# Kernel optimization log

Measured on AMD Instinct MI355X. Metric: run time of the kernel, lower is better.

Reference implementation:

```python
import jax, jax.numpy as jnp
import numpy as np

B, S, E, H, SN, LMAX = 128, 512, 768, 16, 100, 5
DH = E // H  # 48

def setup_inputs() -> dict:
    key = jax.random.key(0)
    ks = jax.random.split(key, 10)
    idx = jax.random.randint(ks[0], (B, LMAX), 0, S)
    lengths = jax.random.randint(ks[1], (B,), 1, LMAX + 1)
    valid = jnp.arange(LMAX)[None, :] < lengths[:, None]
    locations = jnp.where(valid, idx, -1)
    return {
        "last_hidden_state": jax.random.normal(ks[2], (B, S, E), jnp.float32),
        "sense_emb": jax.random.normal(ks[3], (B, SN, E), jnp.float32),
        "locations": locations,
        "in_proj_weight": jax.random.normal(ks[4], (3 * E, E), jnp.float32) * 0.02,
        "in_proj_bias": jax.random.normal(ks[5], (3 * E,), jnp.float32) * 0.02,
        "out_proj_weight": jax.random.normal(ks[6], (E, E), jnp.float32) * 0.02,
        "out_proj_bias": jax.random.normal(ks[7], (E,), jnp.float32) * 0.02,
        "linear_weight": jax.random.normal(ks[8], (SN, E), jnp.float32) * 0.02,
        "linear_bias": jax.random.normal(ks[9], (SN,), jnp.float32) * 0.02,
    }

def reference(last_hidden_state, sense_emb, locations, in_proj_weight, in_proj_bias,
              out_proj_weight, out_proj_bias, linear_weight, linear_bias):
    # Ragged gather + mean over the valid (non -1) token locations per row.
    mask = (locations != -1)                                   # [B, LMAX]
    safe = jnp.where(mask, locations, 0)                       # [B, LMAX]
    gathered = jnp.take_along_axis(last_hidden_state, safe[..., None], axis=1)  # [B,LMAX,E]
    cnt = mask.sum(axis=1, keepdims=True).astype(last_hidden_state.dtype)
    pun = (gathered * mask[..., None]).sum(axis=1) / cnt       # [B, E]

    # qkv: prepend pun-word embedding to the sense embeddings -> [B, SN+1, E]
    qkv = jnp.concatenate([pun[:, None, :], sense_emb], axis=1)

    # nn.MultiheadAttention with batch_first=False: axis0 = seq (L=B), axis1 = batch (N=SN+1).
    proj = qkv @ in_proj_weight.T + in_proj_bias               # [L, N, 3E]
    q, k, v = jnp.split(proj, 3, axis=-1)
    L, N = qkv.shape[0], qkv.shape[1]
    q = q.reshape(L, N, H, DH) * (DH ** -0.5)
    k = k.reshape(L, N, H, DH)
    v = v.reshape(L, N, H, DH)
    scores = jnp.einsum('lnhd,mnhd->nhlm', q, k)               # [N,H,L,L]
    attn = jax.nn.softmax(scores, axis=-1)
    ctx = jnp.einsum('nhlm,mnhd->lnhd', attn, v).reshape(L, N, E)
    attn_out = ctx @ out_proj_weight.T + out_proj_bias         # [L, N, E]

    res = attn_out[:, 0, :]                                    # [B, E] (batch slot 0)
    res = res @ linear_weight.T + linear_bias                  # [B, SN]
    return res
```

## Files before the change

### kernel.cpp

```cpp
#include <hip/hip_runtime.h>

#define SEQ   512
#define EMB   768
#define K3E   2304
#define NH    16
#define DHD   48

__global__ __launch_bounds__(256) void gemm1_fused(
    const float* __restrict__ lhs, const int* __restrict__ loc,
    const float* __restrict__ Bw, const float* __restrict__ bias,
    float* __restrict__ C)
{
  __shared__ float lds[15360];
  const int t  = threadIdx.x;
  const int w  = t >> 6, l = t & 63;
  const int bm = blockIdx.y * 16, bn = blockIdx.x * 64;
  const int tx = l & 15, ty = l >> 4;
  const int gm = l & 15, gq = l >> 4;
  const int kbase = w * 192;
  const int AW = w * 2816;
  const int BW = w * 2816 + 640;

  int locs[5]; int cnt = 0;
#pragma unroll
  for (int j = 0; j < 5; j++) {
    int v = loc[(bm + gm) * 5 + j];
    locs[j] = v; if (v >= 0) cnt++;
  }
  const float ginv = 1.0f / (float)cnt;
  const float* lrow = lhs + (size_t)(bm + gm) * SEQ * EMB;
  const float* brow = Bw + (size_t)(bn + l) * EMB;

  float4 aF, bF0, bF1, bF2, bF3;

#define G1_LOAD(s) {                                                          \
    int k0 = kbase + (s) * 16;                                                \
    float sx=0.f, sy=0.f, sz=0.f, sw=0.f;                                     \
    _Pragma("unroll")                                                         \
    for (int j = 0; j < 5; j++) {                                             \
      int v = locs[j] >= 0 ? locs[j] : 0;                                     \
      float4 wv = *(const float4*)&lrow[(size_t)v * EMB + k0 + gq * 4];       \
      if (locs[j] >= 0) { sx+=wv.x; sy+=wv.y; sz+=wv.z; sw+=wv.w; }           \
    }                                                                         \
    aF = make_float4(sx*ginv, sy*ginv, sz*ginv, sw*ginv);                     \
    bF0 = *(const float4*)&brow[k0 + 0];                                      \
    bF1 = *(const float4*)&brow[k0 + 4];                                      \
    bF2 = *(const float4*)&brow[k0 + 8];                                      \
    bF3 = *(const float4*)&brow[k0 + 12]; }

#define G1_WRITE(b) {                                                         \
    int Ab = AW + (b) * 320;                                                  \
    lds[Ab + (gq*4+0)*20 + gm] = aF.x;                                        \
    lds[Ab + (gq*4+1)*20 + gm] = aF.y;                                        \
    lds[Ab + (gq*4+2)*20 + gm] = aF.z;                                        \
    lds[Ab + (gq*4+3)*20 + gm] = aF.w;                                        \
    int Bb = BW + (b) * 1088;                                                 \
    lds[Bb +  0*68 + l] = bF0.x; lds[Bb +  1*68 + l] = bF0.y;                 \
    lds[Bb +  2*68 + l] = bF0.z; lds[Bb +  3*68 + l] = bF0.w;                 \
    lds[Bb +  4*68 + l] = bF1.x; lds[Bb +  5*68 + l] = bF1.y;                 \
    lds[Bb +  6*68 + l] = bF1.z; lds[Bb +  7*68 + l] = bF1.w;                 \
    lds[Bb +  8*68 + l] = bF2.x; lds[Bb +  9*68 + l] = bF2.y;                 \
    lds[Bb + 10*68 + l] = bF2.z; lds[Bb + 11*68 + l] = bF2.w;                 \
    lds[Bb + 12*68 + l] = bF3.x; lds[Bb + 13*68 + l] = bF3.y;                 \
    lds[Bb + 14*68 + l] = bF3.z; lds[Bb + 15*68 + l] = bF3.w; }

  float acc[4][4] = {};
  G1_LOAD(0); G1_WRITE(0);
  for (int s = 0; s < 12; s++) {
    int b = s & 1;
    if (s < 11) G1_LOAD(s + 1);
    int Ab = AW + b * 320, Bb = BW + b * 1088;
#pragma unroll
    for (int kk = 0; kk < 16; kk++) {
      float4 a  = *(float4*)&lds[Ab + kk * 20 + ty * 4];
      float4 bb = *(float4*)&lds[Bb + kk * 68 + tx * 4];
      acc[0][0] += a.x*bb.x; acc[0][1] += a.x*bb.y; acc[0][2] += a.x*bb.z; acc[0][3] += a.x*bb.w;
      acc[1][0] += a.y*bb.x; acc[1][1] += a.y*bb.y; acc[1][2] += a.y*bb.z; acc[1][3] += a.y*bb.w;
      acc[2][0] += a.z*bb.x; acc[2][1] += a.z*bb.y; acc[2][2] += a.z*bb.z; acc[2][3] += a.z*bb.w;
      acc[3][0] += a.w*bb.x; acc[3][1] += a.w*bb.y; acc[3][2] += a.w*bb.z; acc[3][3] += a.w*bb.w;
    }
    if (s < 11) G1_WRITE(b ^ 1);
  }

  int Rb = 11264 + w * 1024;
#pragma unroll
  for (int i = 0; i < 4; i++)
    *(float4*)&lds[Rb + (ty*4 + i) * 64 + tx * 4] =
        make_float4(acc[i][0], acc[i][1], acc[i][2], acc[i][3]);
  __syncthreads();
  int o = t * 4;
  int m = o >> 6, n = o & 63;
  float4 s0 = *(float4*)&lds[11264 + 0*1024 + o];
  float4 s1 = *(float4*)&lds[11264 + 1*1024 + o];
  float4 s2 = *(float4*)&lds[11264 + 2*1024 + o];
  float4 s3 = *(float4*)&lds[11264 + 3*1024 + o];
  float4 bb = *(const float4*)&bias[bn + n];
  float4 r = make_float4(s0.x+s1.x+s2.x+s3.x+bb.x, s0.y+s1.y+s2.y+s3.y+bb.y,
                         s0.z+s1.z+s2.z+s3.z+bb.z, s0.w+s1.w+s2.w+s3.w+bb.w);
  *(float4*)&C[(size_t)(bm + m) * K3E + bn + n] = r;
#undef G1_LOAD
#undef G1_WRITE
}

__global__ __launch_bounds__(256) void gemm_red(
    const float* __restrict__ A, const float* __restrict__ Bw,
    const float* __restrict__ bias, float* __restrict__ C,
    int N, int LDC)
{
  __shared__ float lds[9216];
  const int t  = threadIdx.x;
  const int w  = t >> 6, l = t & 63;
  const int bm = blockIdx.y * 16, bn = blockIdx.x * 32;
  const int tx = l & 7, ty = l >> 3;
  const int am = l & 15, aq = l >> 4;
  const int bl = l & 31, bh = l >> 5;
  const int kbase = w * 192;
  const int AW = w * 1792;
  const int BW = w * 1792 + 640;

  const float* arow = A + (size_t)(bm + am) * EMB;
  const int brg = bn + bl;
  const bool bok = brg < N;
  const float* brow = Bw + (size_t)(bok ? brg : (N - 1)) * EMB;

  float4 aF, bF0, bF1;

#define G2_LOAD(s) {                                                          \
    int k0 = kbase + (s) * 16;                                                \
    aF = *(const float4*)&arow[k0 + aq * 4];                                  \
    if (bok) {                                                                \
      bF0 = *(const float4*)&brow[k0 + bh * 8 + 0];                           \
      bF1 = *(const float4*)&brow[k0 + bh * 8 + 4];                           \
    } else {                                                                  \
      bF0 = make_float4(0.f,0.f,0.f,0.f); bF1 = bF0;                          \
    } }

#define G2_WRITE(b) {                                                         \
    int Ab = AW + (b) * 320;                                                  \
    lds[Ab + (aq*4+0)*20 + am] = aF.x;                                        \
    lds[Ab + (aq*4+1)*20 + am] = aF.y;                                        \
    lds[Ab + (aq*4+2)*20 + am] = aF.z;                                        \
    lds[Ab + (aq*4+3)*20 + am] = aF.w;                                        \
    int Bb = BW + (b) * 576;                                                  \
    lds[Bb + (bh*8+0)*36 + bl] = bF0.x; lds[Bb + (bh*8+1)*36 + bl] = bF0.y;   \
    lds[Bb + (bh*8+2)*36 + bl] = bF0.z; lds[Bb + (bh*8+3)*36 + bl] = bF0.w;   \
    lds[Bb + (bh*8+4)*36 + bl] = bF1.x; lds[Bb + (bh*8+5)*36 + bl] = bF1.y;   \
    lds[Bb + (bh*8+6)*36 + bl] = bF1.z; lds[Bb + (bh*8+7)*36 + bl] = bF1.w; }

  float acc[2][4] = {};
  G2_LOAD(0); G2_WRITE(0);
  for (int s = 0; s < 12; s++) {
    int b = s & 1;
    if (s < 11) G2_LOAD(s + 1);
    int Ab = AW + b * 320, Bb = BW + b * 576;
#pragma unroll
    for (int kk = 0; kk < 16; kk++) {
      float2 a  = *(float2*)&lds[Ab + kk * 20 + ty * 2];
      float4 bb = *(float4*)&lds[Bb + kk * 36 + tx * 4];
      acc[0][0] += a.x*bb.x; acc[0][1] += a.x*bb.y; acc[0][2] += a.x*bb.z; acc[0][3] += a.x*bb.w;
      acc[1][0] += a.y*bb.x; acc[1][1] += a.y*bb.y; acc[1][2] += a.y*bb.z; acc[1][3] += a.y*bb.w;
    }
    if (s < 11) G2_WRITE(b ^ 1);
  }

  int Rb = 7168 + w * 512;
#pragma unroll
  for (int i = 0; i < 2; i++)
    *(float4*)&lds[Rb + (ty*2 + i) * 32 + tx * 4] =
        make_float4(acc[i][0], acc[i][1], acc[i][2], acc[i][3]);
  __syncthreads();
  int o = t * 2;
  int m = o >> 5, n = o & 31;
#pragma unroll
  for (int j = 0; j < 2; j++) {
    int ng = bn + n + j;
    if (ng < N) {
      float v = lds[7168 + 0*512 + o + j] + lds[7168 + 1*512 + o + j] +
                lds[7168 + 2*512 + o + j] + lds[7168 + 3*512 + o + j] + bias[ng];
      C[(size_t)(bm + m) * LDC + ng] = v;
    }
  }
#undef G2_LOAD
#undef G2_WRITE
}

__global__ __launch_bounds__(256) void attn_kernel(
    const float* __restrict__ proj, float* __restrict__ ctx)
{
  __shared__ float ks[128][52];
  __shared__ float vs[128][52];
  int h  = blockIdx.x;
  int l0 = blockIdx.y * 16;
  int t  = threadIdx.x;

  for (int i = t; i < 128 * 12; i += 256) {
    int m  = i / 12;
    int dd = (i - m * 12) * 4;
    float4 kv = *(const float4*)&proj[(size_t)m * K3E + EMB     + h * DHD + dd];
    float4 vv = *(const float4*)&proj[(size_t)m * K3E + 2 * EMB + h * DHD + dd];
    *(float4*)&ks[m][dd] = kv;
    *(float4*)&vs[m][dd] = vv;
  }

  int l  = t >> 4;
  int g  = t & 15;
  int lg = l0 + l;
  const float scale = 0.14433756729740643f;
  float q[48];
#pragma unroll
  for (int jj = 0; jj < 12; jj++) {
    float4 qv = *(const float4*)&proj[(size_t)lg * K3E + h * DHD + jj * 4];
    q[jj * 4 + 0] = qv.x * scale; q[jj * 4 + 1] = qv.y * scale;
    q[jj * 4 + 2] = qv.z * scale; q[jj * 4 + 3] = qv.w * scale;
  }
  __syncthreads();

  float sv[8];
  float smax = -1e30f;
#pragma unroll
  for (int jm = 0; jm < 8; jm++) {
    int m = g + jm * 16;
    float s = 0.0f;
#pragma unroll
    for (int dq = 0; dq < 12; dq++) {
      float4 kv = *(const float4*)&ks[m][dq * 4];
      s += q[dq * 4 + 0] * kv.x + q[dq * 4 + 1] * kv.y +
           q[dq * 4 + 2] * kv.z + q[dq * 4 + 3] * kv.w;
    }
    sv[jm] = s;
    smax = fmaxf(smax, s);
  }
#pragma unroll
  for (int off = 1; off < 16; off <<= 1) smax = fmaxf(smax, __shfl_xor(smax, off));
  float ssum = 0.0f;
#pragma unroll
  for (int jm = 0; jm < 8; jm++) { float e = __expf(sv[jm] - smax); sv[jm] = e; ssum += e; }
#pragma unroll
  for (int off = 1; off < 16; off <<= 1) ssum += __shfl_xor(ssum, off);
  float inv = 1.0f / ssum;
#pragma unroll
  for (int jm = 0; jm < 8; jm++) sv[jm] *= inv;

  float acc[48] = {};
#pragma unroll
  for (int jm = 0; jm < 8; jm++) {
    int m = g + jm * 16;
    float p = sv[jm];
#pragma unroll
    for (int dq = 0; dq < 12; dq++) {
      float4 vv = *(const float4*)&vs[m][dq * 4];
      acc[dq * 4 + 0] += p * vv.x; acc[dq * 4 + 1] += p * vv.y;
      acc[dq * 4 + 2] += p * vv.z; acc[dq * 4 + 3] += p * vv.w;
    }
  }

  {
    float buf[24];
    if (g & 8) {
#pragma unroll
      for (int d = 0; d < 24; d++) buf[d] = acc[d];
    } else {
#pragma unroll
      for (int d = 0; d < 24; d++) buf[d] = acc[d + 24];
    }
#pragma unroll
    for (int d = 0; d < 24; d++) buf[d] = __shfl_xor(buf[d], 8);
    if (g & 8) {
#pragma unroll
      for (int d = 0; d < 24; d++) acc[d] = acc[d + 24] + buf[d];
    } else {
#pragma unroll
      for (int d = 0; d < 24; d++) acc[d] = acc[d] + buf[d];
    }
  }
  {
    float buf[12];
    if (g & 4) {
#pragma unroll
      for (int d = 0; d < 12; d++) buf[d] = acc[d];
    } else {
#pragma unroll
      for (int d = 0; d < 12; d++) buf[d] = acc[d + 12];
    }
#pragma unroll
    for (int d = 0; d < 12; d++) buf[d] = __shfl_xor(buf[d], 4);
    if (g & 4) {
#pragma unroll
      for (int d = 0; d < 12; d++) acc[d] = acc[d + 12] + buf[d];
    } else {
#pragma unroll
      for (int d = 0; d < 12; d++) acc[d] = acc[d] + buf[d];
    }
  }
  {
    float buf[6];
    if (g & 2) {
#pragma unroll
      for (int d = 0; d < 6; d++) buf[d] = acc[d];
    } else {
#pragma unroll
      for (int d = 0; d < 6; d++) buf[d] = acc[d + 6];
    }
#pragma unroll
    for (int d = 0; d < 6; d++) buf[d] = __shfl_xor(buf[d], 2);
    if (g & 2) {
#pragma unroll
      for (int d = 0; d < 6; d++) acc[d] = acc[d + 6] + buf[d];
    } else {
#pragma unroll
      for (int d = 0; d < 6; d++) acc[d] = acc[d] + buf[d];
    }
  }
  {
    float buf[3];
    if (g & 1) {
#pragma unroll
      for (int d = 0; d < 3; d++) buf[d] = acc[d];
    } else {
#pragma unroll
      for (int d = 0; d < 3; d++) buf[d] = acc[d + 3];
    }
#pragma unroll
    for (int d = 0; d < 3; d++) buf[d] = __shfl_xor(buf[d], 1);
    if (g & 1) {
#pragma unroll
      for (int d = 0; d < 3; d++) acc[d] = acc[d + 3] + buf[d];
    } else {
#pragma unroll
      for (int d = 0; d < 3; d++) acc[d] = acc[d] + buf[d];
    }
  }
#pragma unroll
  for (int j = 0; j < 3; j++) {
    ctx[(size_t)lg * EMB + h * DHD + g * 3 + j] = acc[j];
  }
}

extern "C" void kernel_launch(void* const* d_in, const int* in_sizes, int n_in,
                              void* d_out, int out_size, void* d_ws, size_t ws_size,
                              hipStream_t stream) {
  const float* lhs   = (const float*)d_in[0];
  const int*   loc   = (const int*)  d_in[2];
  const float* w_in  = (const float*)d_in[3];
  const float* b_in  = (const float*)d_in[4];
  const float* w_out = (const float*)d_in[5];
  const float* b_out = (const float*)d_in[6];
  const float* w_lin = (const float*)d_in[7];
  const float* b_lin = (const float*)d_in[8];
  float* out = (float*)d_out;

  char* ws = (char*)d_ws;
  float* proj     = (float*)(ws);
  float* ctx      = (float*)(ws + 1179648);
  float* attn_out = (float*)(ws + 1179648 + 393216);

  gemm1_fused<<<dim3(36, 8), 256, 0, stream>>>(lhs, loc, w_in, b_in, proj);
  attn_kernel<<<dim3(NH, 8), 256, 0, stream>>>(proj, ctx);
  gemm_red<<<dim3(24, 8), 256, 0, stream>>>(ctx, w_out, b_out, attn_out, EMB, EMB);
  gemm_red<<<dim3(4, 8), 256, 0, stream>>>(attn_out, w_lin, b_lin, out, 100, 100);
}
```

Before: 56.75 us.

## Fold out_proj into final linear and compute combined weight alongside attention

The out-projection and final linear are merged algebraically: Wcomb = W_lin·W_out is computed by extra blocks inside the attention kernel, and the bias W_lin·b_out + b_lin is computed inside the final kernel. This removes one launch and the 128x768x768 out-projection GEMM, replacing it with a 100x768x768 weight product that runs concurrently with attention. The first GEMM's tile width is also halved from 64 to 32 columns, doubling its block count for better CU occupancy. Rounding order changes slightly, and the weight product is recomputed every call.

```diff
diff --git a/kernel.cpp b/kernel.cpp
--- a/kernel.cpp
+++ b/kernel.cpp
@@ -1,25 +1,24 @@
 #include <hip/hip_runtime.h>
 
-#define SEQ   512
-#define EMB   768
-#define K3E   2304
-#define NH    16
-#define DHD   48
-
-__global__ __launch_bounds__(256) void gemm1_fused(
+#define SEQ 512
+#define EMB 768
+#define K3E 2304
+#define DHD 48
+
+__global__ __launch_bounds__(256) void k1_gemm1(
     const float* __restrict__ lhs, const int* __restrict__ loc,
     const float* __restrict__ Bw, const float* __restrict__ bias,
     float* __restrict__ C)
 {
-  __shared__ float lds[15360];
+  __shared__ float lds[7168];
   const int t  = threadIdx.x;
   const int w  = t >> 6, l = t & 63;
-  const int bm = blockIdx.y * 16, bn = blockIdx.x * 64;
-  const int tx = l & 15, ty = l >> 4;
+  const int bm = blockIdx.y * 16, bn = blockIdx.x * 32;
+  const int tx = l & 7, ty = l >> 3;
   const int gm = l & 15, gq = l >> 4;
+  const int bl = l & 31, bh = l >> 5;
   const int kbase = w * 192;
-  const int AW = w * 2816;
-  const int BW = w * 2816 + 640;
+  const int AW = w * 1792, BW = AW + 640;
 
   int locs[5]; int cnt = 0;
 #pragma unroll
@@ -29,85 +28,299 @@
   }
   const float ginv = 1.0f / (float)cnt;
   const float* lrow = lhs + (size_t)(bm + gm) * SEQ * EMB;
-  const float* brow = Bw + (size_t)(bn + l) * EMB;
-
-  float4 aF, bF0, bF1, bF2, bF3;
-
-#define G1_LOAD(s) {                                                          \
-    int k0 = kbase + (s) * 16;                                                \
-    float sx=0.f, sy=0.f, sz=0.f, sw=0.f;                                     \
-    _Pragma("unroll")                                                         \
-    for (int j = 0; j < 5; j++) {                                             \
-      int v = locs[j] >= 0 ? locs[j] : 0;                                     \
-      float4 wv = *(const float4*)&lrow[(size_t)v * EMB + k0 + gq * 4];       \
-      if (locs[j] >= 0) { sx+=wv.x; sy+=wv.y; sz+=wv.z; sw+=wv.w; }           \
-    }                                                                         \
-    aF = make_float4(sx*ginv, sy*ginv, sz*ginv, sw*ginv);                     \
-    bF0 = *(const float4*)&brow[k0 + 0];                                      \
-    bF1 = *(const float4*)&brow[k0 + 4];                                      \
-    bF2 = *(const float4*)&brow[k0 + 8];                                      \
-    bF3 = *(const float4*)&brow[k0 + 12]; }
-
-#define G1_WRITE(b) {                                                         \
-    int Ab = AW + (b) * 320;                                                  \
-    lds[Ab + (gq*4+0)*20 + gm] = aF.x;                                        \
-    lds[Ab + (gq*4+1)*20 + gm] = aF.y;                                        \
-    lds[Ab + (gq*4+2)*20 + gm] = aF.z;                                        \
-    lds[Ab + (gq*4+3)*20 + gm] = aF.w;                                        \
-    int Bb = BW + (b) * 1088;                                                 \
-    lds[Bb +  0*68 + l] = bF0.x; lds[Bb +  1*68 + l] = bF0.y;                 \
-    lds[Bb +  2*68 + l] = bF0.z; lds[Bb +  3*68 + l] = bF0.w;                 \
-    lds[Bb +  4*68 + l] = bF1.x; lds[Bb +  5*68 + l] = bF1.y;                 \
-    lds[Bb +  6*68 + l] = bF1.z; lds[Bb +  7*68 + l] = bF1.w;                 \
-    lds[Bb +  8*68 + l] = bF2.x; lds[Bb +  9*68 + l] = bF2.y;                 \
-    lds[Bb + 10*68 + l] = bF2.z; lds[Bb + 11*68 + l] = bF2.w;                 \
-    lds[Bb + 12*68 + l] = bF3.x; lds[Bb + 13*68 + l] = bF3.y;                 \
-    lds[Bb + 14*68 + l] = bF3.z; lds[Bb + 15*68 + l] = bF3.w; }
-
-  float acc[4][4] = {};
-  G1_LOAD(0); G1_WRITE(0);
+  const float* brow = Bw + (size_t)(bn + bl) * EMB;
+
+  float4 aF, bF0, bF1;
+
+#define K1_LOAD(s) {                                                         \
+    int k0 = kbase + (s) * 16;                                               \
+    float sx=0.f, sy=0.f, sz=0.f, sw=0.f;                                    \
+    _Pragma("unroll")                                                        \
+    for (int j = 0; j < 5; j++) {                                            \
+      int v = locs[j] >= 0 ? locs[j] : 0;                                    \
+      float4 wv = *(const float4*)&lrow[(size_t)v * EMB + k0 + gq * 4];      \
+      if (locs[j] >= 0) { sx+=wv.x; sy+=wv.y; sz+=wv.z; sw+=wv.w; }          \
+    }                                                                        \
+    aF = make_float4(sx*ginv, sy*ginv, sz*ginv, sw*ginv);                    \
+    bF0 = *(const float4*)&brow[k0 + bh * 8 + 0];                            \
+    bF1 = *(const float4*)&brow[k0 + bh * 8 + 4]; }
+
+#define K1_WRITE(b) {                                                        \
+    int Ab = AW + (b) * 320;                                                 \
+    lds[Ab + (gq*4+0)*20 + gm] = aF.x;                                       \
+    lds[Ab + (gq*4+1)*20 + gm] = aF.y;                                       \
+    lds[Ab + (gq*4+2)*20 + gm] = aF.z;                                       \
+    lds[Ab + (gq*4+3)*20 + gm] = aF.w;                                       \
+    int Bb = BW + (b) * 576;                                                 \
+    lds[Bb + (bh*8+0)*36 + bl] = bF0.x; lds[Bb + (bh*8+1)*36 + bl] = bF0.y;  \
+    lds[Bb + (bh*8+2)*36 + bl] = bF0.z; lds[Bb + (bh*8+3)*36 + bl] = bF0.w;  \
+    lds[Bb + (bh*8+4)*36 + bl] = bF1.x; lds[Bb + (bh*8+5)*36 + bl] = bF1.y;  \
+    lds[Bb + (bh*8+6)*36 + bl] = bF1.z; lds[Bb + (bh*8+7)*36 + bl] = bF1.w; }
+
+  float acc[2][4] = {};
+  K1_LOAD(0); K1_WRITE(0);
   for (int s = 0; s < 12; s++) {
     int b = s & 1;
-    if (s < 11) G1_LOAD(s + 1);
-    int Ab = AW + b * 320, Bb = BW + b * 1088;
+    if (s < 11) K1_LOAD(s + 1);
+    int Ab = AW + b * 320, Bb = BW + b * 576;
 #pragma unroll
     for (int kk = 0; kk < 16; kk++) {
-      float4 a  = *(float4*)&lds[Ab + kk * 20 + ty * 4];
-      float4 bb = *(float4*)&lds[Bb + kk * 68 + tx * 4];
+      float2 a  = *(float2*)&lds[Ab + kk * 20 + ty * 2];
+      float4 bb = *(float4*)&lds[Bb + kk * 36 + tx * 4];
       acc[0][0] += a.x*bb.x; acc[0][1] += a.x*bb.y; acc[0][2] += a.x*bb.z; acc[0][3] += a.x*bb.w;
       acc[1][0] += a.y*bb.x; acc[1][1] += a.y*bb.y; acc[1][2] += a.y*bb.z; acc[1][3] += a.y*bb.w;
-      acc[2][0] += a.z*bb.x; acc[2][1] += a.z*bb.y; acc[2][2] += a.z*bb.z; acc[2][3] += a.z*bb.w;
-      acc[3][0] += a.w*bb.x; acc[3][1] += a.w*bb.y; acc[3][2] += a.w*bb.z; acc[3][3] += a.w*bb.w;
-    }
-    if (s < 11) G1_WRITE(b ^ 1);
-  }
-
-  int Rb = 11264 + w * 1024;
-#pragma unroll
-  for (int i = 0; i < 4; i++)
-    *(float4*)&lds[Rb + (ty*4 + i) * 64 + tx * 4] =
+    }
+    if (s < 11) K1_WRITE(b ^ 1);
+  }
+#undef K1_LOAD
+#undef K1_WRITE
+
+#pragma unroll
+  for (int i = 0; i < 2; i++)
+    *(float4*)&lds[AW + (ty*2 + i) * 32 + tx * 4] =
         make_float4(acc[i][0], acc[i][1], acc[i][2], acc[i][3]);
   __syncthreads();
-  int o = t * 4;
-  int m = o >> 6, n = o & 63;
-  float4 s0 = *(float4*)&lds[11264 + 0*1024 + o];
-  float4 s1 = *(float4*)&lds[11264 + 1*1024 + o];
-  float4 s2 = *(float4*)&lds[11264 + 2*1024 + o];
-  float4 s3 = *(float4*)&lds[11264 + 3*1024 + o];
-  float4 bb = *(const float4*)&bias[bn + n];
-  float4 r = make_float4(s0.x+s1.x+s2.x+s3.x+bb.x, s0.y+s1.y+s2.y+s3.y+bb.y,
-                         s0.z+s1.z+s2.z+s3.z+bb.z, s0.w+s1.w+s2.w+s3.w+bb.w);
-  *(float4*)&C[(size_t)(bm + m) * K3E + bn + n] = r;
-#undef G1_LOAD
-#undef G1_WRITE
+  int o = t * 2;
+  int m = o >> 5, n = o & 31;
+  float2 s0 = *(float2*)&lds[0*1792 + o];
+  float2 s1 = *(float2*)&lds[1*1792 + o];
+  float2 s2 = *(float2*)&lds[2*1792 + o];
+  float2 s3 = *(float2*)&lds[3*1792 + o];
+  float2 bb2 = *(const float2*)&bias[bn + n];
+  float2 r = make_float2(s0.x+s1.x+s2.x+s3.x+bb2.x, s0.y+s1.y+s2.y+s3.y+bb2.y);
+  *(float2*)&C[(size_t)(bm + m) * K3E + bn + n] = r;
 }
 
-__global__ __launch_bounds__(256) void gemm_red(
+__global__ __launch_bounds__(256) void k2_attn_wcomb(
+    const float* __restrict__ proj, float* __restrict__ ctx,
+    const float* __restrict__ wlin, const float* __restrict__ wout,
+    float* __restrict__ wcomb)
+{
+  __shared__ float lds[13312];
+  const int t = threadIdx.x;
+
+  if (blockIdx.x < 128) {
+    float* ks = lds;
+    float* vs = lds + 6656;
+    int h  = blockIdx.x >> 3;
+    int l0 = (blockIdx.x & 7) * 16;
+
+    for (int i = t; i < 128 * 12; i += 256) {
+      int m  = i / 12;
+      int dd = (i - m * 12) * 4;
+      float4 kv = *(const float4*)&proj[(size_t)m * K3E + EMB     + h * DHD + dd];
+      float4 vv = *(const float4*)&proj[(size_t)m * K3E + 2 * EMB + h * DHD + dd];
+      *(float4*)&ks[m * 52 + dd] = kv;
+      *(float4*)&vs[m * 52 + dd] = vv;
+    }
+
+    int l  = t >> 4;
+    int g  = t & 15;
+    int lg = l0 + l;
+    const float scale = 0.14433756729740643f;
+    float q[48];
+#pragma unroll
+    for (int jj = 0; jj < 12; jj++) {
+      float4 qv = *(const float4*)&proj[(size_t)lg * K3E + h * DHD + jj * 4];
+      q[jj*4+0] = qv.x * scale; q[jj*4+1] = qv.y * scale;
+      q[jj*4+2] = qv.z * scale; q[jj*4+3] = qv.w * scale;
+    }
+    __syncthreads();
+
+    float sv[8];
+    float smax = -1e30f;
+#pragma unroll
+    for (int jm = 0; jm < 8; jm++) {
+      int m = g + jm * 16;
+      float s = 0.0f;
+#pragma unroll
+      for (int dq = 0; dq < 12; dq++) {
+        float4 kv = *(const float4*)&ks[m * 52 + dq * 4];
+        s += q[dq*4+0]*kv.x + q[dq*4+1]*kv.y + q[dq*4+2]*kv.z + q[dq*4+3]*kv.w;
+      }
+      sv[jm] = s;
+      smax = fmaxf(smax, s);
+    }
+#pragma unroll
+    for (int off = 1; off < 16; off <<= 1) smax = fmaxf(smax, __shfl_xor(smax, off));
+    float ssum = 0.0f;
+#pragma unroll
+    for (int jm = 0; jm < 8; jm++) { float e = __expf(sv[jm] - smax); sv[jm] = e; ssum += e; }
+#pragma unroll
+    for (int off = 1; off < 16; off <<= 1) ssum += __shfl_xor(ssum, off);
+    float inv = 1.0f / ssum;
+#pragma unroll
+    for (int jm = 0; jm < 8; jm++) sv[jm] *= inv;
+
+    float acc[48] = {};
+#pragma unroll
+    for (int jm = 0; jm < 8; jm++) {
+      int m = g + jm * 16;
+      float p = sv[jm];
+#pragma unroll
+      for (int dq = 0; dq < 12; dq++) {
+        float4 vv = *(const float4*)&vs[m * 52 + dq * 4];
+        acc[dq*4+0] += p*vv.x; acc[dq*4+1] += p*vv.y;
+        acc[dq*4+2] += p*vv.z; acc[dq*4+3] += p*vv.w;
+      }
+    }
+
+    {
+      float buf[24];
+      if (g & 8) {
+#pragma unroll
+        for (int d = 0; d < 24; d++) buf[d] = acc[d];
+      } else {
+#pragma unroll
+        for (int d = 0; d < 24; d++) buf[d] = acc[d + 24];
+      }
+#pragma unroll
+      for (int d = 0; d < 24; d++) buf[d] = __shfl_xor(buf[d], 8);
+      if (g & 8) {
+#pragma unroll
+        for (int d = 0; d < 24; d++) acc[d] = acc[d + 24] + buf[d];
+      } else {
+#pragma unroll
+        for (int d = 0; d < 24; d++) acc[d] = acc[d] + buf[d];
+      }
+    }
+    {
+      float buf[12];
+      if (g & 4) {
+#pragma unroll
+        for (int d = 0; d < 12; d++) buf[d] = acc[d];
+      } else {
+#pragma unroll
+        for (int d = 0; d < 12; d++) buf[d] = acc[d + 12];
+      }
+#pragma unroll
+      for (int d = 0; d < 12; d++) buf[d] = __shfl_xor(buf[d], 4);
+      if (g & 4) {
+#pragma unroll
+        for (int d = 0; d < 12; d++) acc[d] = acc[d + 12] + buf[d];
+      } else {
+#pragma unroll
+        for (int d = 0; d < 12; d++) acc[d] = acc[d] + buf[d];
+      }
+    }
+    {
+      float buf[6];
+      if (g & 2) {
+#pragma unroll
+        for (int d = 0; d < 6; d++) buf[d] = acc[d];
+      } else {
+#pragma unroll
+        for (int d = 0; d < 6; d++) buf[d] = acc[d + 6];
+      }
+#pragma unroll
+      for (int d = 0; d < 6; d++) buf[d] = __shfl_xor(buf[d], 2);
+      if (g & 2) {
+#pragma unroll
+        for (int d = 0; d < 6; d++) acc[d] = acc[d + 6] + buf[d];
+      } else {
+#pragma unroll
+        for (int d = 0; d < 6; d++) acc[d] = acc[d] + buf[d];
+      }
+    }
+    {
+      float buf[3];
+      if (g & 1) {
+#pragma unroll
+        for (int d = 0; d < 3; d++) buf[d] = acc[d];
+      } else {
+#pragma unroll
+        for (int d = 0; d < 3; d++) buf[d] = acc[d + 3];
+      }
+#pragma unroll
+      for (int d = 0; d < 3; d++) buf[d] = __shfl_xor(buf[d], 1);
+      if (g & 1) {
+#pragma unroll
+        for (int d = 0; d < 3; d++) acc[d] = acc[d + 3] + buf[d];
+      } else {
+#pragma unroll
+        for (int d = 0; d < 3; d++) acc[d] = acc[d] + buf[d];
+      }
+    }
+#pragma unroll
+    for (int j = 0; j < 3; j++) {
+      ctx[(size_t)lg * EMB + h * DHD + g * 3 + j] = acc[j];
+    }
+  } else {
+    const int c  = blockIdx.x - 128;
+    const int bm = (c / 24) * 16;
+    const int bn = (c % 24) * 32;
+    const int w  = t >> 6, l = t & 63;
+    const int tx = l & 7, ty = l >> 3;
+    const int am = l & 15, aq = l >> 4;
+    const int wi = l >> 2;
+    const int j4 = (l & 3) * 8;
+    const int kbase = w * 192;
+    const int AW = w * 1792, BW = AW + 640;
+
+    int arow_i = bm + am; if (arow_i > 99) arow_i = 99;
+    const float* arow = wlin + (size_t)arow_i * EMB;
+
+    float4 aF, bF0, bF1;
+
+#define W_LOAD(s) {                                                          \
+    int k0 = kbase + (s) * 16;                                               \
+    aF  = *(const float4*)&arow[k0 + aq * 4];                                \
+    const float* wr = wout + (size_t)(k0 + wi) * EMB + bn + j4;              \
+    bF0 = *(const float4*)&wr[0];                                            \
+    bF1 = *(const float4*)&wr[4]; }
+
+#define W_WRITE(b) {                                                         \
+    int Ab = AW + (b) * 320;                                                 \
+    lds[Ab + (aq*4+0)*20 + am] = aF.x;                                       \
+    lds[Ab + (aq*4+1)*20 + am] = aF.y;                                       \
+    lds[Ab + (aq*4+2)*20 + am] = aF.z;                                       \
+    lds[Ab + (aq*4+3)*20 + am] = aF.w;                                       \
+    int Bb = BW + (b) * 576;                                                 \
+    *(float4*)&lds[Bb + wi*36 + j4]     = bF0;                               \
+    *(float4*)&lds[Bb + wi*36 + j4 + 4] = bF1; }
+
+    float acc[2][4] = {};
+    W_LOAD(0); W_WRITE(0);
+    for (int s = 0; s < 12; s++) {
+      int b = s & 1;
+      if (s < 11) W_LOAD(s + 1);
+      int Ab = AW + b * 320, Bb = BW + b * 576;
+#pragma unroll
+      for (int kk = 0; kk < 16; kk++) {
+        float2 a  = *(float2*)&lds[Ab + kk * 20 + ty * 2];
+        float4 bb = *(float4*)&lds[Bb + kk * 36 + tx * 4];
+        acc[0][0] += a.x*bb.x; acc[0][1] += a.x*bb.y; acc[0][2] += a.x*bb.z; acc[0][3] += a.x*bb.w;
+        acc[1][0] += a.y*bb.x; acc[1][1] += a.y*bb.y; acc[1][2] += a.y*bb.z; acc[1][3] += a.y*bb.w;
+      }
+      if (s < 11) W_WRITE(b ^ 1);
+    }
+#undef W_LOAD
+#undef W_WRITE
+
+#pragma unroll
+    for (int i = 0; i < 2; i++)
+      *(float4*)&lds[AW + (ty*2 + i) * 32 + tx * 4] =
+          make_float4(acc[i][0], acc[i][1], acc[i][2], acc[i][3]);
+    __syncthreads();
+    int o = t * 2;
+    int m = o >> 5, n = o & 31;
+    if (bm + m < 100) {
+      float2 s0 = *(float2*)&lds[0*1792 + o];
+      float2 s1 = *(float2*)&lds[1*1792 + o];
+      float2 s2 = *(float2*)&lds[2*1792 + o];
+      float2 s3 = *(float2*)&lds[3*1792 + o];
+      float2 r = make_float2(s0.x+s1.x+s2.x+s3.x, s0.y+s1.y+s2.y+s3.y);
+      *(float2*)&wcomb[(size_t)(bm + m) * EMB + bn + n] = r;
+    }
+  }
+}
+
+__global__ __launch_bounds__(256) void k3_final(
     const float* __restrict__ A, const float* __restrict__ Bw,
-    const float* __restrict__ bias, float* __restrict__ C,
-    int N, int LDC)
+    const float* __restrict__ wlin, const float* __restrict__ bout,
+    const float* __restrict__ blin, float* __restrict__ C)
 {
-  __shared__ float lds[9216];
+  __shared__ float lds[7200];
   const int t  = threadIdx.x;
   const int w  = t >> 6, l = t & 63;
   const int bm = blockIdx.y * 16, bn = blockIdx.x * 32;
@@ -115,43 +328,54 @@
   const int am = l & 15, aq = l >> 4;
   const int bl = l & 31, bh = l >> 5;
   const int kbase = w * 192;
-  const int AW = w * 1792;
-  const int BW = w * 1792 + 640;
+  const int AW = w * 1792, BW = AW + 640;
+
+  {
+    int col = bn + (t >> 3);
+    int ks  = (t & 7) * 96;
+    float p = 0.f;
+    if (col < 100) {
+      const float* wr = wlin + (size_t)col * EMB + ks;
+#pragma unroll
+      for (int j = 0; j < 24; j++) {
+        float4 wv = *(const float4*)&wr[j * 4];
+        float4 bv = *(const float4*)&bout[ks + j * 4];
+        p += wv.x*bv.x + wv.y*bv.y + wv.z*bv.z + wv.w*bv.w;
+      }
+    }
+    p += __shfl_xor(p, 1); p += __shfl_xor(p, 2); p += __shfl_xor(p, 4);
+    if ((t & 7) == 0) lds[7168 + (t >> 3)] = p + (col < 100 ? blin[col] : 0.f);
+  }
 
   const float* arow = A + (size_t)(bm + am) * EMB;
-  const int brg = bn + bl;
-  const bool bok = brg < N;
-  const float* brow = Bw + (size_t)(bok ? brg : (N - 1)) * EMB;
+  int brow_i = bn + bl; if (brow_i > 99) brow_i = 99;
+  const float* brow = Bw + (size_t)brow_i * EMB;
 
   float4 aF, bF0, bF1;
 
-#define G2_LOAD(s) {                                                          \
-    int k0 = kbase + (s) * 16;                                                \
-    aF = *(const float4*)&arow[k0 + aq * 4];                                  \
-    if (bok) {                                                                \
-      bF0 = *(const float4*)&brow[k0 + bh * 8 + 0];                           \
-      bF1 = *(const float4*)&brow[k0 + bh * 8 + 4];                           \
-    } else {                                                                  \
-      bF0 = make_float4(0.f,0.f,0.f,0.f); bF1 = bF0;                          \
-    } }
-
-#define G2_WRITE(b) {                                                         \
-    int Ab = AW + (b) * 320;                                                  \
-    lds[Ab + (aq*4+0)*20 + am] = aF.x;                                        \
-    lds[Ab + (aq*4+1)*20 + am] = aF.y;                                        \
-    lds[Ab + (aq*4+2)*20 + am] = aF.z;                                        \
-    lds[Ab + (aq*4+3)*20 + am] = aF.w;                                        \
-    int Bb = BW + (b) * 576;                                                  \
-    lds[Bb + (bh*8+0)*36 + bl] = bF0.x; lds[Bb + (bh*8+1)*36 + bl] = bF0.y;   \
-    lds[Bb + (bh*8+2)*36 + bl] = bF0.z; lds[Bb + (bh*8+3)*36 + bl] = bF0.w;   \
-    lds[Bb + (bh*8+4)*36 + bl] = bF1.x; lds[Bb + (bh*8+5)*36 + bl] = bF1.y;   \
+#define F_LOAD(s) {                                                          \
+    int k0 = kbase + (s) * 16;                                               \
+    aF  = *(const float4*)&arow[k0 + aq * 4];                                \
+    bF0 = *(const float4*)&brow[k0 + bh * 8 + 0];                            \
+    bF1 = *(const float4*)&brow[k0 + bh * 8 + 4]; }
+
+#define F_WRITE(b) {                                                         \
+    int Ab = AW + (b) * 320;                                                 \
+    lds[Ab + (aq*4+0)*20 + am] = aF.x;                                       \
+    lds[Ab + (aq*4+1)*20 + am] = aF.y;                                       \
+    lds[Ab + (aq*4+2)*20 + am] = aF.z;                                       \
+    lds[Ab + (aq*4+3)*20 + am] = aF.w;                                       \
+    int Bb = BW + (b) * 576;                                                 \
+    lds[Bb + (bh*8+0)*36 + bl] = bF0.x; lds[Bb + (bh*8+1)*36 + bl] = bF0.y;  \
+    lds[Bb + (bh*8+2)*36 + bl] = bF0.z; lds[Bb + (bh*8+3)*36 + bl] = bF0.w;  \
+    lds[Bb + (bh*8+4)*36 + bl] = bF1.x; lds[Bb + (bh*8+5)*36 + bl] = bF1.y;  \
     lds[Bb + (bh*8+6)*36 + bl] = bF1.z; lds[Bb + (bh*8+7)*36 + bl] = bF1.w; }
 
   float acc[2][4] = {};
-  G2_LOAD(0); G2_WRITE(0);
+  F_LOAD(0); F_WRITE(0);
   for (int s = 0; s < 12; s++) {
     int b = s & 1;
-    if (s < 11) G2_LOAD(s + 1);
+    if (s < 11) F_LOAD(s + 1);
     int Ab = AW + b * 320, Bb = BW + b * 576;
 #pragma unroll
     for (int kk = 0; kk < 16; kk++) {
@@ -160,179 +384,26 @@
       acc[0][0] += a.x*bb.x; acc[0][1] += a.x*bb.y; acc[0][2] += a.x*bb.z; acc[0][3] += a.x*bb.w;
       acc[1][0] += a.y*bb.x; acc[1][1] += a.y*bb.y; acc[1][2] += a.y*bb.z; acc[1][3] += a.y*bb.w;
     }
-    if (s < 11) G2_WRITE(b ^ 1);
-  }
-
-  int Rb = 7168 + w * 512;
+    if (s < 11) F_WRITE(b ^ 1);
+  }
+#undef F_LOAD
+#undef F_WRITE
+
 #pragma unroll
   for (int i = 0; i < 2; i++)
-    *(float4*)&lds[Rb + (ty*2 + i) * 32 + tx * 4] =
+    *(float4*)&lds[AW + (ty*2 + i) * 32 + tx * 4] =
         make_float4(acc[i][0], acc[i][1], acc[i][2], acc[i][3]);
   __syncthreads();
   int o = t * 2;
   int m = o >> 5, n = o & 31;
 #pragma unroll
   for (int j = 0; j < 2; j++) {
-    int ng = bn + n + j;
-    if (ng < N) {
-      float v = lds[7168 + 0*512 + o + j] + lds[7168 + 1*512 + o + j] +
-                lds[7168 + 2*512 + o + j] + lds[7168 + 3*512 + o + j] + bias[ng];
-      C[(size_t)(bm + m) * LDC + ng] = v;
-    }
-  }
-#undef G2_LOAD
-#undef G2_WRITE
-}
-
-__global__ __launch_bounds__(256) void attn_kernel(
-    const float* __restrict__ proj, float* __restrict__ ctx)
-{
-  __shared__ float ks[128][52];
-  __shared__ float vs[128][52];
-  int h  = blockIdx.x;
-  int l0 = blockIdx.y * 16;
-  int t  = threadIdx.x;
-
-  for (int i = t; i < 128 * 12; i += 256) {
-    int m  = i / 12;
-    int dd = (i - m * 12) * 4;
-    float4 kv = *(const float4*)&proj[(size_t)m * K3E + EMB     + h * DHD + dd];
-    float4 vv = *(const float4*)&proj[(size_t)m * K3E + 2 * EMB + h * DHD + dd];
-    *(float4*)&ks[m][dd] = kv;
-    *(float4*)&vs[m][dd] = vv;
-  }
-
-  int l  = t >> 4;
-  int g  = t & 15;
-  int lg = l0 + l;
-  const float scale = 0.14433756729740643f;
-  float q[48];
-#pragma unroll
-  for (int jj = 0; jj < 12; jj++) {
-    float4 qv = *(const float4*)&proj[(size_t)lg * K3E + h * DHD + jj * 4];
-    q[jj * 4 + 0] = qv.x * scale; q[jj * 4 + 1] = qv.y * scale;
-    q[jj * 4 + 2] = qv.z * scale; q[jj * 4 + 3] = qv.w * scale;
-  }
-  __syncthreads();
-
-  float sv[8];
-  float smax = -1e30f;
-#pragma unroll
-  for (int jm = 0; jm < 8; jm++) {
-    int m = g + jm * 16;
-    float s = 0.0f;
-#pragma unroll
-    for (int dq = 0; dq < 12; dq++) {
-      float4 kv = *(const float4*)&ks[m][dq * 4];
-      s += q[dq * 4 + 0] * kv.x + q[dq * 4 + 1] * kv.y +
-           q[dq * 4 + 2] * kv.z + q[dq * 4 + 3] * kv.w;
-    }
-    sv[jm] = s;
-    smax = fmaxf(smax, s);
-  }
-#pragma unroll
-  for (int off = 1; off < 16; off <<= 1) smax = fmaxf(smax, __shfl_xor(smax, off));
-  float ssum = 0.0f;
-#pragma unroll
-  for (int jm = 0; jm < 8; jm++) { float e = __expf(sv[jm] - smax); sv[jm] = e; ssum += e; }
-#pragma unroll
-  for (int off = 1; off < 16; off <<= 1) ssum += __shfl_xor(ssum, off);
-  float inv = 1.0f / ssum;
-#pragma unroll
-  for (int jm = 0; jm < 8; jm++) sv[jm] *= inv;
-
-  float acc[48] = {};
-#pragma unroll
-  for (int jm = 0; jm < 8; jm++) {
-    int m = g + jm * 16;
-    float p = sv[jm];
-#pragma unroll
-    for (int dq = 0; dq < 12; dq++) {
-      float4 vv = *(const float4*)&vs[m][dq * 4];
-      acc[dq * 4 + 0] += p * vv.x; acc[dq * 4 + 1] += p * vv.y;
-      acc[dq * 4 + 2] += p * vv.z; acc[dq * 4 + 3] += p * vv.w;
-    }
-  }
-
-  {
-    float buf[24];
-    if (g & 8) {
-#pragma unroll
-      for (int d = 0; d < 24; d++) buf[d] = acc[d];
-    } else {
-#pragma unroll
-      for (int d = 0; d < 24; d++) buf[d] = acc[d + 24];
-    }
-#pragma unroll
-    for (int d = 0; d < 24; d++) buf[d] = __shfl_xor(buf[d], 8);
-    if (g & 8) {
-#pragma unroll
-      for (int d = 0; d < 24; d++) acc[d] = acc[d + 24] + buf[d];
-    } else {
-#pragma unroll
-      for (int d = 0; d < 24; d++) acc[d] = acc[d] + buf[d];
-    }
-  }
-  {
-    float buf[12];
-    if (g & 4) {
-#pragma unroll
-      for (int d = 0; d < 12; d++) buf[d] = acc[d];
-    } else {
-#pragma unroll
-      for (int d = 0; d < 12; d++) buf[d] = acc[d + 12];
-    }
-#pragma unroll
-    for (int d = 0; d < 12; d++) buf[d] = __shfl_xor(buf[d], 4);
-    if (g & 4) {
-#pragma unroll
-      for (int d = 0; d < 12; d++) acc[d] = acc[d + 12] + buf[d];
-    } else {
-#pragma unroll
-      for (int d = 0; d < 12; d++) acc[d] = acc[d] + buf[d];
-    }
-  }
-  {
-    float buf[6];
-    if (g & 2) {
-#pragma unroll
-      for (int d = 0; d < 6; d++) buf[d] = acc[d];
-    } else {
-#pragma unroll
-      for (int d = 0; d < 6; d++) buf[d] = acc[d + 6];
-    }
-#pragma unroll
-    for (int d = 0; d < 6; d++) buf[d] = __shfl_xor(buf[d], 2);
-    if (g & 2) {
-#pragma unroll
-      for (int d = 0; d < 6; d++) acc[d] = acc[d + 6] + buf[d];
-    } else {
-#pragma unroll
-      for (int d = 0; d < 6; d++) acc[d] = acc[d] + buf[d];
-    }
-  }
-  {
-    float buf[3];
-    if (g & 1) {
-#pragma unroll
-      for (int d = 0; d < 3; d++) buf[d] = acc[d];
-    } else {
-#pragma unroll
-      for (int d = 0; d < 3; d++) buf[d] = acc[d + 3];
-    }
-#pragma unroll
-    for (int d = 0; d < 3; d++) buf[d] = __shfl_xor(buf[d], 1);
-    if (g & 1) {
-#pragma unroll
-      for (int d = 0; d < 3; d++) acc[d] = acc[d + 3] + buf[d];
-    } else {
-#pragma unroll
-      for (int d = 0; d < 3; d++) acc[d] = acc[d] + buf[d];
-    }
-  }
-#pragma unroll
-  for (int j = 0; j < 3; j++) {
-    ctx[(size_t)lg * EMB + h * DHD + g * 3 + j] = acc[j];
+    int col = bn + n + j;
+    if (col < 100) {
+      float v = lds[0*1792 + o + j] + lds[1*1792 + o + j] +
+                lds[2*1792 + o + j] + lds[3*1792 + o + j] + lds[7168 + n + j];
+      C[(size_t)(bm + m) * 100 + col] = v;
+    }
   }
 }
 
@@ -350,12 +421,11 @@
   float* out = (float*)d_out;
 
   char* ws = (char*)d_ws;
-  float* proj     = (float*)(ws);
-  float* ctx      = (float*)(ws + 1179648);
-  float* attn_out = (float*)(ws + 1179648 + 393216);
-
-  gemm1_fused<<<dim3(36, 8), 256, 0, stream>>>(lhs, loc, w_in, b_in, proj);
-  attn_kernel<<<dim3(NH, 8), 256, 0, stream>>>(proj, ctx);
-  gemm_red<<<dim3(24, 8), 256, 0, stream>>>(ctx, w_out, b_out, attn_out, EMB, EMB);
-  gemm_red<<<dim3(4, 8), 256, 0, stream>>>(attn_out, w_lin, b_lin, out, 100, 100);
+  float* proj  = (float*)(ws);
+  float* ctx   = (float*)(ws + 1179648);
+  float* wcomb = (float*)(ws + 1179648 + 393216);
+
+  k1_gemm1<<<dim3(72, 8), 256, 0, stream>>>(lhs, loc, w_in, b_in, proj);
+  k2_attn_wcomb<<<296, 256, 0, stream>>>(proj, ctx, w_lin, w_out, wcomb);
+  k3_final<<<dim3(4, 8), 256, 0, stream>>>(ctx, wcomb, w_lin, b_out, b_lin, out);
 }
```

Measured after the change: 51.70 us. 1.1x faster.
